# Kernel tuning notes

Hardware: AMD Instinct MI355X
Metric: run time of the kernel (lower is better)

## Reference

```python
import jax, jax.numpy as jnp
import numpy as np

T, B, D = 1024, 8, 1024
H, DH, FF = 16, 64, 4096
BG = 0.1  # GRU gating bias constant
SCALE = 1.0 / DH ** 0.5


def layer_norm(x, g, b, eps=1e-5):
    mu = jnp.mean(x, axis=-1, keepdims=True)
    var = jnp.var(x, axis=-1, keepdims=True)
    return (x - mu) * jax.lax.rsqrt(var + eps) * g + b


def gru_gate(x, y, W, U, bz):
    # W, U: [3, D, D] stacking (r, z, g) projections; bz: Uz bias
    r = jax.nn.sigmoid(y @ W[0] + x @ U[0])
    z = jax.nn.sigmoid(y @ W[1] + x @ U[1] + bz - BG)
    h = jnp.tanh(y @ W[2] + r * (x @ U[2]))
    return (1.0 - z) * x + z * h


def setup_inputs() -> dict:
    key = jax.random.key(0)
    ks = jax.random.split(key, 16)
    s = 0.02
    inp = {
        "x": jax.random.normal(ks[0], (T, B, D), jnp.float32),
        "Wq": jax.random.normal(ks[1], (D, H * DH), jnp.float32) * s,
        "Wk": jax.random.normal(ks[2], (D, H * DH), jnp.float32) * s,
        "Wv": jax.random.normal(ks[3], (D, H * DH), jnp.float32) * s,
        "Wo": jax.random.normal(ks[4], (H * DH, D), jnp.float32) * s,
        "ln1_g": jnp.ones((D,), jnp.float32),
        "ln1_b": jnp.zeros((D,), jnp.float32),
        "W1": jax.random.normal(ks[5], (D, FF), jnp.float32) * s,
        "b1": jnp.zeros((FF,), jnp.float32),
        "W2": jax.random.normal(ks[6], (FF, D), jnp.float32) * s,
        "b2": jnp.zeros((D,), jnp.float32),
        "ln2_g": jnp.ones((D,), jnp.float32),
        "ln2_b": jnp.zeros((D,), jnp.float32),
        "gate1_W": jax.random.normal(ks[7], (3, D, D), jnp.float32) * s,
        "gate1_U": jax.random.normal(ks[8], (3, D, D), jnp.float32) * s,
        "gate1_bz": jnp.zeros((D,), jnp.float32),
        "gate2_W": jax.random.normal(ks[9], (3, D, D), jnp.float32) * s,
        "gate2_U": jax.random.normal(ks[10], (3, D, D), jnp.float32) * s,
        "gate2_bz": jnp.zeros((D,), jnp.float32),
        "attn_mask": jnp.triu(jnp.ones((T, T), bool), k=1),  # causal: mask j > i
    }
    return inp


def reference(x, Wq, Wk, Wv, Wo, ln1_g, ln1_b, W1, b1, W2, b2,
              ln2_g, ln2_b, gate1_W, gate1_U, gate1_bz,
              gate2_W, gate2_U, gate2_bz, attn_mask):
    # --- multihead attention (pre_lnorm=True) ---
    xn = layer_norm(x, ln1_g, ln1_b)                     # [T,B,D]
    q = (xn @ Wq).reshape(T, B, H, DH)
    k = (xn @ Wk).reshape(T, B, H, DH)
    v = (xn @ Wv).reshape(T, B, H, DH)
    scores = jnp.einsum('ibhd,jbhd->ijbh', q, k) * SCALE  # [T,T,B,H]
    scores = jnp.where(attn_mask[:, :, None, None], -jnp.inf, scores)
    probs = jax.nn.softmax(scores, axis=1)
    attn = jnp.einsum('ijbh,jbhd->ibhd', probs, v).reshape(T, B, H * DH)
    src2 = attn @ Wo                                      # [T,B,D]
    # --- GRU gate 1 ---
    src = gru_gate(x, src2, gate1_W, gate1_U, gate1_bz)
    # --- positionwise FFN (pre_lnorm=True) ---
    sn = layer_norm(src, ln2_g, ln2_b)
    ff = jax.nn.relu(sn @ W1 + b1) @ W2 + b2
    # --- GRU gate 2 ---
    return gru_gate(src, ff, gate2_W, gate2_U, gate2_bz)
```

## Files before the change

kernel.cpp:

```cpp
#include <hip/hip_runtime.h>
#include <hip/hip_bf16.h>

#define T_  1024
#define B_  8
#define D_  1024
#define H_  16
#define DH_ 64
#define FF_ 4096
#define MROWS (T_*B_)

typedef __attribute__((ext_vector_type(8))) short short8;
typedef __attribute__((ext_vector_type(4))) float f32x4;
typedef __attribute__((ext_vector_type(4))) unsigned short us4;
typedef __attribute__((ext_vector_type(4))) unsigned int  u32x4;

__device__ __forceinline__ unsigned short f2b(float f){
  unsigned int u = __builtin_bit_cast(unsigned int, f);
  u += 0x7FFFu + ((u >> 16) & 1u);
  return (unsigned short)(u >> 16);
}
__device__ __forceinline__ float b2f(unsigned short h){
  unsigned int u = ((unsigned int)h) << 16;
  return __builtin_bit_cast(float, u);
}

__device__ __forceinline__ void glds16(const unsigned short* g, unsigned short* l){
  __builtin_amdgcn_global_load_lds(
    (const __attribute__((address_space(1))) unsigned int*)g,
    (__attribute__((address_space(3))) unsigned int*)l, 16, 0, 0);
}

enum { FRELU=1 };

__global__ __launch_bounds__(256) void gemm_bf16(
    const unsigned short* __restrict__ A1, const unsigned short* __restrict__ A2,
    int K1, long lda,
    const unsigned short* __restrict__ Bt, long ldb,
    unsigned short* __restrict__ C, long ldc,
    const float* __restrict__ bias, int K, int flags)
{
  constexpr int BM = 128, BK = 32;
  __shared__ unsigned short As[2][BM*BK];
  __shared__ unsigned short Bs[2][BM*BK];

  int t = threadIdx.x, w = t >> 6, l = t & 63;

  int nx = gridDim.x;
  int nwg = nx * gridDim.y;
  int lin = blockIdx.y*nx + blockIdx.x;
  if (!(nwg & 7)) lin = (lin & 7)*(nwg >> 3) + (lin >> 3);
  int bx = lin % nx, by = lin / nx;
  int m0 = by*BM, n0 = bx*BM;

  int arow = t >> 2, acol = (t & 3) * 8;
  const unsigned short* a1p = A1 + (long)(m0 + arow)*lda + acol;
  const unsigned short* a2p = A2 + (long)(m0 + arow)*lda + acol - K1;
  const unsigned short* bp  = Bt + (long)(n0 + arow)*ldb + acol;

  auto stage = [&](int buf, int k0){
    const unsigned short* ap = (k0 < K1) ? a1p : a2p;
    glds16(ap + k0,          &As[buf][      w*512]);
    glds16(ap + 64*lda + k0, &As[buf][2048 + w*512]);
    glds16(bp + k0,          &Bs[buf][      w*512]);
    glds16(bp + 64*ldb + k0, &Bs[buf][2048 + w*512]);
  };

  f32x4 acc[4][4];
  #pragma unroll
  for (int m=0;m<4;m++)
    #pragma unroll
    for (int n=0;n<4;n++) acc[m][n] = (f32x4){0.f,0.f,0.f,0.f};

  int wm = (w >> 1) * 64, wn = (w & 1) * 64;
  int fr = l & 15, fk = (l >> 4) * 8;
  int nk = K / BK;

  stage(0, 0);
  __syncthreads();

  for (int kt = 0; kt < nk; ++kt){
    int cur = kt & 1;
    if (kt + 1 < nk) stage(cur ^ 1, (kt+1)*BK);

    short8 af[4], bf[4];
    #pragma unroll
    for (int m=0;m<4;m++) af[m] = *(const short8*)&As[cur][(wm + m*16 + fr)*BK + fk];
    #pragma unroll
    for (int n=0;n<4;n++) bf[n] = *(const short8*)&Bs[cur][(wn + n*16 + fr)*BK + fk];
    #pragma unroll
    for (int m=0;m<4;m++)
      #pragma unroll
      for (int n=0;n<4;n++)
        acc[m][n] = __builtin_amdgcn_mfma_f32_16x16x32_bf16(af[m], bf[n], acc[m][n], 0, 0, 0);

    __syncthreads();
  }

  int r0 = m0 + wm + ((l >> 4) << 2);
  int c0 = n0 + wn + fr;
  #pragma unroll
  for (int m=0;m<4;m++)
    #pragma unroll
    for (int n=0;n<4;n++){
      int col = c0 + n*16;
      float bv = bias ? bias[col] : 0.f;
      #pragma unroll
      for (int j=0;j<4;j++){
        float v = acc[m][n][j] + bv;
        if (flags & FRELU) v = v > 0.f ? v : 0.f;
        C[(long)(r0 + m*16 + j)*ldc + col] = f2b(v);
      }
    }
}

__global__ __launch_bounds__(256) void flash_attn(
  const unsigned short* __restrict__ qkv, const unsigned short* __restrict__ vT,
  unsigned short* __restrict__ O)
{
  int p = blockIdx.x, z = blockIdx.y;
  int b = z >> 4, h = z & 15;
  const unsigned short* Vz = vT + (long)z*DH_*T_;

  __shared__ unsigned short Ks[64*64];
  __shared__ unsigned short Vs[64*64];
  __shared__ unsigned short Ps[4][32][72];

  int t = threadIdx.x, w = t >> 6, l = t & 63;
  int fr = l & 15, fg = l >> 4;
  int srow = t >> 2, sc = (t & 3) * 16;

  for (int rep = 0; rep < 2; ++rep){
    int qt = rep ? (7 - p) : p;
    int q0 = qt*128 + w*32;

    short8 qf[2][2];
    #pragma unroll
    for (int m=0;m<2;m++)
      #pragma unroll
      for (int ks=0;ks<2;ks++)
        qf[m][ks] = *(const short8*)(qkv + ((long)(q0 + m*16 + fr)*B_ + b)*3072 + h*DH_ + ks*32 + fg*8);

    f32x4 oacc[2][4];
    float mr[2][4], lr[2][4];
    #pragma unroll
    for (int m=0;m<2;m++){
      #pragma unroll
      for (int n=0;n<4;n++) oacc[m][n] = (f32x4){0.f,0.f,0.f,0.f};
      #pragma unroll
      for (int j=0;j<4;j++){ mr[m][j] = -1e30f; lr[m][j] = 0.f; }
    }

    int nkv = (qt + 1) * 2;
    for (int kt = 0; kt < nkv; ++kt){
      int kv0 = kt * 64;
      __syncthreads();
      {
        const unsigned short* kg = qkv + ((long)(kv0+srow)*B_ + b)*3072 + 1024 + h*DH_ + sc;
        const unsigned short* vg = Vz + (long)srow*T_ + kv0 + sc;
        int rb = srow*128, sw = (srow & 7) << 4;
        *(u32x4*)((char*)Ks + ((rb + sc*2     ) ^ sw)) = *(const u32x4*)(kg);
        *(u32x4*)((char*)Ks + ((rb + sc*2 + 16) ^ sw)) = *(const u32x4*)(kg + 8);
        *(u32x4*)((char*)Vs + ((rb + sc*2     ) ^ sw)) = *(const u32x4*)(vg);
        *(u32x4*)((char*)Vs + ((rb + sc*2 + 16) ^ sw)) = *(const u32x4*)(vg + 8);
      }
      __syncthreads();

      if (kv0 <= q0 + 31){
        f32x4 sacc[2][4];
        #pragma unroll
        for (int m=0;m<2;m++)
          #pragma unroll
          for (int n=0;n<4;n++) sacc[m][n] = (f32x4){0.f,0.f,0.f,0.f};
        __builtin_amdgcn_s_setprio(1);
        #pragma unroll
        for (int ks=0;ks<2;ks++){
          short8 kf[4];
          #pragma unroll
          for (int n=0;n<4;n++){
            int r = n*16 + fr;
            kf[n] = *(const short8*)((const char*)Ks + ((r*128 + ks*64 + fg*16) ^ ((r & 7) << 4)));
          }
          #pragma unroll
          for (int m=0;m<2;m++)
            #pragma unroll
            for (int n=0;n<4;n++)
              sacc[m][n] = __builtin_amdgcn_mfma_f32_16x16x32_bf16(qf[m][ks], kf[n], sacc[m][n], 0,0,0);
        }
        __builtin_amdgcn_s_setprio(0);

        #pragma unroll
        for (int m=0;m<2;m++)
          #pragma unroll
          for (int j=0;j<4;j++){
            int qg = q0 + m*16 + fg*4 + j;
            float vmax = -1e30f;
            #pragma unroll
            for (int n=0;n<4;n++){
              int kg = kv0 + n*16 + fr;
              float s = (kg <= qg) ? sacc[m][n][j]*0.125f : -1e30f;
              sacc[m][n][j] = s;
              vmax = fmaxf(vmax, s);
            }
            #pragma unroll
            for (int msk=1; msk<16; msk<<=1) vmax = fmaxf(vmax, __shfl_xor(vmax, msk));
            float mnew = fmaxf(mr[m][j], vmax);
            float sc_o = __expf(mr[m][j] - mnew);
            mr[m][j] = mnew;
            float rsum = 0.f;
            #pragma unroll
            for (int n=0;n<4;n++){
              float pv = __expf(sacc[m][n][j] - mnew);
              sacc[m][n][j] = pv;
              rsum += pv;
            }
            #pragma unroll
            for (int msk=1; msk<16; msk<<=1) rsum += __shfl_xor(rsum, msk);
            lr[m][j] = lr[m][j]*sc_o + rsum;
            #pragma unroll
            for (int n=0;n<4;n++) oacc[m][n][j] *= sc_o;
          }

        #pragma unroll
        for (int m=0;m<2;m++)
          #pragma unroll
          for (int n=0;n<4;n++)
            #pragma unroll
            for (int j=0;j<4;j++)
              Ps[w][m*16 + fg*4 + j][n*16 + fr] = f2b(sacc[m][n][j]);

        __builtin_amdgcn_s_setprio(1);
        #pragma unroll
        for (int ks=0;ks<2;ks++){
          short8 pf[2], vf[4];
          #pragma unroll
          for (int m=0;m<2;m++) pf[m] = *(const short8*)&Ps[w][m*16+fr][ks*32+fg*8];
          #pragma unroll
          for (int n=0;n<4;n++){
            int r = n*16 + fr;
            vf[n] = *(const short8*)((const char*)Vs + ((r*128 + ks*64 + fg*16) ^ ((r & 7) << 4)));
          }
          #pragma unroll
          for (int m=0;m<2;m++)
            #pragma unroll
            for (int n=0;n<4;n++)
              oacc[m][n] = __builtin_amdgcn_mfma_f32_16x16x32_bf16(pf[m], vf[n], oacc[m][n], 0,0,0);
        }
        __builtin_amdgcn_s_setprio(0);
      }
    }

    #pragma unroll
    for (int m=0;m<2;m++)
      #pragma unroll
      for (int j=0;j<4;j++){
        float inv = 1.f / lr[m][j];
        long i = q0 + m*16 + fg*4 + j;
        #pragma unroll
        for (int n=0;n<4;n++)
          O[(i*B_ + b)*(long)D_ + h*DH_ + n*16 + fr] = f2b(oacc[m][n][j] * inv);
      }
  }
}

__global__ __launch_bounds__(256) void ln_bf16(const float* __restrict__ X,
    const float* __restrict__ g, const float* __restrict__ bta,
    unsigned short* __restrict__ out)
{
  long row = blockIdx.x;
  int t = threadIdx.x;
  f32x4 xv = ((const f32x4*)(X + row*D_))[t];
  float s = xv[0]+xv[1]+xv[2]+xv[3];
  float q = xv[0]*xv[0]+xv[1]*xv[1]+xv[2]*xv[2]+xv[3]*xv[3];
  #pragma unroll
  for (int o=32;o;o>>=1){ s += __shfl_xor(s,o); q += __shfl_xor(q,o); }
  __shared__ float rs[4], rq[4];
  int w = t >> 6;
  if ((t & 63) == 0){ rs[w]=s; rq[w]=q; }
  __syncthreads();
  s = rs[0]+rs[1]+rs[2]+rs[3];
  q = rq[0]+rq[1]+rq[2]+rq[3];
  float mean = s * (1.f/D_);
  float var  = q * (1.f/D_) - mean*mean;
  float rstd = rsqrtf(var + 1e-5f);
  f32x4 gv = ((const f32x4*)g)[t];
  f32x4 bv = ((const f32x4*)bta)[t];
  us4 o;
  #pragma unroll
  for (int jj=0;jj<4;jj++) o[jj] = f2b((xv[jj]-mean)*rstd*gv[jj] + bv[jj]);
  ((us4*)(out + row*D_))[t] = o;
}

__global__ __launch_bounds__(256) void tr_f2b(const float* __restrict__ src,
    unsigned short* __restrict__ dst, int N, long ldd)
{
  __shared__ float tile[32][33];
  int k0 = blockIdx.x*32, n0 = blockIdx.y*32;
  int tx = threadIdx.x & 31, ty = threadIdx.x >> 5;
  #pragma unroll
  for (int i=0;i<4;i++)
    tile[ty+i*8][tx] = src[(long)(k0+ty+i*8)*N + n0 + tx];
  __syncthreads();
  #pragma unroll
  for (int i=0;i<4;i++)
    dst[(long)(n0+ty+i*8)*ldd + k0 + tx] = f2b(tile[tx][ty+i*8]);
}

__global__ __launch_bounds__(256) void build_vT(const unsigned short* __restrict__ vsrc,
                                                unsigned short* __restrict__ vT)
{
  __shared__ unsigned short tile[32][33];
  int z = blockIdx.z, b = z >> 4, h = z & 15;
  int t0 = blockIdx.x*32, d0 = blockIdx.y*32;
  int tx = threadIdx.x & 31, ty = threadIdx.x >> 5;
  #pragma unroll
  for (int i=0;i<4;i++)
    tile[ty+i*8][tx] = vsrc[((long)(t0+ty+i*8)*B_ + b)*3072 + h*DH_ + d0 + tx];
  __syncthreads();
  #pragma unroll
  for (int i=0;i<4;i++)
    vT[(long)z*DH_*T_ + (long)(d0+ty+i*8)*T_ + t0 + tx] = tile[tx][ty+i*8];
}

__global__ __launch_bounds__(256) void cast_f2b(const float* __restrict__ src,
                                                unsigned short* __restrict__ dst)
{
  long i = ((long)blockIdx.x*256 + threadIdx.x)*4;
  f32x4 v = *(const f32x4*)(src + i);
  us4 o;
  #pragma unroll
  for (int jj=0;jj<4;jj++) o[jj] = f2b(v[jj]);
  *(us4*)(dst + i) = o;
}

__global__ __launch_bounds__(256) void gru_combine(
  const unsigned short* __restrict__ rz,
  const unsigned short* __restrict__ ya, const unsigned short* __restrict__ xb,
  const float* __restrict__ xin, const float* __restrict__ bz,
  float* __restrict__ of, unsigned short* __restrict__ ob)
{
  long i = ((long)blockIdx.x*256 + threadIdx.x)*4;
  long row = i >> 10; int col = (int)(i & 1023);
  us4 r4 = *(const us4*)(rz + row*2048 + col);
  us4 z4 = *(const us4*)(rz + row*2048 + 1024 + col);
  us4 a4 = *(const us4*)(ya + i);
  us4 b4 = *(const us4*)(xb + i);
  f32x4 xv = *(const f32x4*)(xin + i);
  f32x4 bzv = *(const f32x4*)(bz + col);
  f32x4 o;
  #pragma unroll
  for (int jj=0;jj<4;jj++){
    float r = 1.f/(1.f + __expf(-b2f(r4[jj])));
    float z = 1.f/(1.f + __expf(-(b2f(z4[jj]) + bzv[jj] - 0.1f)));
    float h = tanhf(b2f(a4[jj]) + r*b2f(b4[jj]));
    o[jj] = (1.f - z)*xv[jj] + z*h;
  }
  *(f32x4*)(of+i) = o;
  if (ob){
    us4 q;
    #pragma unroll
    for (int jj=0;jj<4;jj++) q[jj] = f2b(o[jj]);
    *(us4*)(ob+i) = q;
  }
}

extern "C" void kernel_launch(void* const* d_in, const int* in_sizes, int n_in,
                              void* d_out, int out_size, void* d_ws, size_t ws_size,
                              hipStream_t stream)
{
  const float* x    = (const float*)d_in[0];
  const float* Wq   = (const float*)d_in[1];
  const float* Wk   = (const float*)d_in[2];
  const float* Wv   = (const float*)d_in[3];
  const float* Wo   = (const float*)d_in[4];
  const float* ln1g = (const float*)d_in[5];
  const float* ln1b = (const float*)d_in[6];
  const float* W1   = (const float*)d_in[7];
  const float* b1   = (const float*)d_in[8];
  const float* W2   = (const float*)d_in[9];
  const float* b2   = (const float*)d_in[10];
  const float* ln2g = (const float*)d_in[11];
  const float* ln2b = (const float*)d_in[12];
  const float* g1W  = (const float*)d_in[13];
  const float* g1U  = (const float*)d_in[14];
  const float* g1bz = (const float*)d_in[15];
  const float* g2W  = (const float*)d_in[16];
  const float* g2U  = (const float*)d_in[17];
  const float* g2bz = (const float*)d_in[18];
  float* out = (float*)d_out;

  const size_t MB = 1u << 20;
  if (ws_size < 144*MB) return;
  char* base = (char*)d_ws;

  unsigned short* W    = (unsigned short*)(base);
  unsigned short* x_bf = (unsigned short*)(base + 16*MB);
  unsigned short* sbf  = (unsigned short*)(base + 32*MB);
  unsigned short* src2 = (unsigned short*)(base + 48*MB);
  unsigned short* qkv  = (unsigned short*)(base + 64*MB);
  unsigned short* vT   = (unsigned short*)(base + 112*MB);
  unsigned short* attn = (unsigned short*)(base + 128*MB);
  unsigned short* xn   = attn;
  unsigned short* rz   = (unsigned short*)(base + 64*MB);
  unsigned short* yab  = (unsigned short*)(base + 96*MB);
  unsigned short* xbb  = (unsigned short*)(base + 112*MB);
  unsigned short* sn   = (unsigned short*)(base + 64*MB);
  unsigned short* ff1  = (unsigned short*)(base + 80*MB);
  unsigned short* ffb  = src2;

  const size_t E1M = 1048576;
  unsigned short* BtRZ = W;
  unsigned short* W2g  = W + 4*E1M;
  unsigned short* U2g  = W + 5*E1M;
  unsigned short* W1T  = W;
  unsigned short* W2T  = W + 4*E1M;
  unsigned short* Wqkv = W;
  unsigned short* WoT  = W + 3*E1M;

  dim3 blk(256);
  auto G = [&](const unsigned short* A1, const unsigned short* A2, int K1, long lda,
               const unsigned short* Bt, long ldb, unsigned short* C, long ldc,
               const float* bias, int M, int N, int K, int flags){
    gemm_bf16<<<dim3(N/128, M/128), blk, 0, stream>>>(A1,A2,K1,lda,Bt,ldb,C,ldc,bias,K,flags);
  };

  tr_f2b<<<dim3(32,32), blk, 0, stream>>>(Wq, Wqkv,          D_, D_);
  tr_f2b<<<dim3(32,32), blk, 0, stream>>>(Wk, Wqkv + 1*E1M,  D_, D_);
  tr_f2b<<<dim3(32,32), blk, 0, stream>>>(Wv, Wqkv + 2*E1M,  D_, D_);
  tr_f2b<<<dim3(32,32), blk, 0, stream>>>(Wo, WoT,           D_, D_);
  cast_f2b<<<dim3(MROWS), blk, 0, stream>>>(x, x_bf);

  ln_bf16<<<dim3(MROWS), blk, 0, stream>>>(x, ln1g, ln1b, xn);
  G(xn, xn, D_, D_, Wqkv, D_, qkv, 3072, nullptr, MROWS, 3072, D_, 0);
  build_vT<<<dim3(32,2,128), blk, 0, stream>>>(qkv + 2048, vT);
  flash_attn<<<dim3(4, B_*H_), blk, 0, stream>>>(qkv, vT, attn);
  G(attn, attn, D_, D_, WoT, D_, src2, D_, nullptr, MROWS, D_, D_, 0);

  tr_f2b<<<dim3(32,32), blk, 0, stream>>>(g1W + 0*E1M, BtRZ,                    D_, 2048);
  tr_f2b<<<dim3(32,32), blk, 0, stream>>>(g1U + 0*E1M, BtRZ + 1024,             D_, 2048);
  tr_f2b<<<dim3(32,32), blk, 0, stream>>>(g1W + 1*E1M, BtRZ + 1024*2048,        D_, 2048);
  tr_f2b<<<dim3(32,32), blk, 0, stream>>>(g1U + 1*E1M, BtRZ + 1024*2048 + 1024, D_, 2048);
  tr_f2b<<<dim3(32,32), blk, 0, stream>>>(g1W + 2*E1M, W2g, D_, D_);
  tr_f2b<<<dim3(32,32), blk, 0, stream>>>(g1U + 2*E1M, U2g, D_, D_);
  G(src2, x_bf, D_, D_, BtRZ, 2048, rz, 2048, nullptr, MROWS, 2048, 2048, 0);
  G(src2, src2, D_, D_, W2g, D_, yab, D_, nullptr, MROWS, D_, D_, 0);
  G(x_bf, x_bf, D_, D_, U2g, D_, xbb, D_, nullptr, MROWS, D_, D_, 0);
  gru_combine<<<dim3(MROWS), blk, 0, stream>>>(rz, yab, xbb, x, g1bz, out, sbf);

  tr_f2b<<<dim3(32,128), blk, 0, stream>>>(W1, W1T, FF_, D_);
  tr_f2b<<<dim3(128,32), blk, 0, stream>>>(W2, W2T, D_, FF_);
  ln_bf16<<<dim3(MROWS), blk, 0, stream>>>(out, ln2g, ln2b, sn);
  G(sn, sn, D_, D_, W1T, D_, ff1, FF_, b1, MROWS, FF_, D_, FRELU);
  G(ff1, ff1, FF_, FF_, W2T, FF_, ffb, D_, b2, MROWS, D_, FF_, 0);

  tr_f2b<<<dim3(32,32), blk, 0, stream>>>(g2W + 0*E1M, BtRZ,                    D_, 2048);
  tr_f2b<<<dim3(32,32), blk, 0, stream>>>(g2U + 0*E1M, BtRZ + 1024,             D_, 2048);
  tr_f2b<<<dim3(32,32), blk, 0, stream>>>(g2W + 1*E1M, BtRZ + 1024*2048,        D_, 2048);
  tr_f2b<<<dim3(32,32), blk, 0, stream>>>(g2U + 1*E1M, BtRZ + 1024*2048 + 1024, D_, 2048);
  tr_f2b<<<dim3(32,32), blk, 0, stream>>>(g2W + 2*E1M, W2g, D_, D_);
  tr_f2b<<<dim3(32,32), blk, 0, stream>>>(g2U + 2*E1M, U2g, D_, D_);
  G(ffb, sbf, D_, D_, BtRZ, 2048, rz, 2048, nullptr, MROWS, 2048, 2048, 0);
  G(ffb, ffb, D_, D_, W2g, D_, yab, D_, nullptr, MROWS, D_, D_, 0);
  G(sbf, sbf, D_, D_, U2g, D_, xbb, D_, nullptr, MROWS, D_, D_, 0);
  gru_combine<<<dim3(MROWS), blk, 0, stream>>>(rz, yab, xbb, out, g2bz, out, nullptr);
}
```

Baseline: 833.3 us.

## Add 256x256-tile triple-buffered GEMM for large-N projections

Adds a second GEMM kernel with 256x256 output tiles, 512 threads (8 waves each computing 128x64), and a three-stage LDS ring using direct global-to-LDS loads in dynamic shared memory. It is used for the wide GEMMs (QKV, GRU r/z, FFN up-projection) to raise arithmetic intensity per tile and keep more loads in flight. The extra register pressure from a 32-tile accumulator and the 96KB of LDS limit occupancy. Grids become smaller, which can hurt load balance on the N=2048 shapes.

```diff
diff --git a/kernel.cpp b/kernel.cpp
--- a/kernel.cpp
+++ b/kernel.cpp
@@ -31,6 +31,116 @@
 }
 
 enum { FRELU=1 };
+
+__global__ __launch_bounds__(512, 2) void gemm256(
+    const unsigned short* __restrict__ A1, const unsigned short* __restrict__ A2,
+    int K1, long lda,
+    const unsigned short* __restrict__ Bt, long ldb,
+    unsigned short* __restrict__ C, long ldc,
+    const float* __restrict__ bias, int K, int flags)
+{
+  constexpr int BM = 256, BK = 32;
+  extern __shared__ char L[];
+
+  int t = threadIdx.x, w = t >> 6, l = t & 63;
+
+  int nx = gridDim.x;
+  int nwg = nx * gridDim.y;
+  int lin = blockIdx.y*nx + blockIdx.x;
+  if (!(nwg & 7)) lin = (lin & 7)*(nwg >> 3) + (lin >> 3);
+  int bx = lin % nx, by = lin / nx;
+  int m0 = by*BM, n0 = bx*BM;
+
+  int srow[2], sce[2];
+  #pragma unroll
+  for (int q=0;q<2;q++){
+    int p  = q*8192 + w*1024 + l*16;
+    int sp = p ^ (((p>>6)&3)<<4);
+    srow[q] = sp >> 6;
+    sce[q]  = (sp & 63) >> 1;
+  }
+
+  auto stage = [&](int buf, int kt){
+    int k0 = kt*BK;
+    const unsigned short* ap; int ko;
+    if (k0 < K1){ ap = A1; ko = k0; } else { ap = A2; ko = k0 - K1; }
+    char* ab = L + buf*32768;
+    char* bb = ab + 16384;
+    #pragma unroll
+    for (int q=0;q<2;q++)
+      glds16(ap + (long)(m0 + srow[q])*lda + ko + sce[q],
+             (unsigned short*)(ab + q*8192 + w*1024));
+    #pragma unroll
+    for (int q=0;q<2;q++)
+      glds16(Bt + (long)(n0 + srow[q])*ldb + k0 + sce[q],
+             (unsigned short*)(bb + q*8192 + w*1024));
+  };
+
+  f32x4 acc[8][4];
+  #pragma unroll
+  for (int m=0;m<8;m++)
+    #pragma unroll
+    for (int n=0;n<4;n++) acc[m][n] = (f32x4){0.f,0.f,0.f,0.f};
+
+  int wr = w >> 2, wc = w & 3;
+  int fr = l & 15, fq = l >> 4;
+  int nk = K / BK;
+
+  stage(0, 0);
+  stage(1, 1);
+  asm volatile("s_waitcnt vmcnt(4)" ::: "memory");
+  __builtin_amdgcn_s_barrier();
+  asm volatile("" ::: "memory");
+
+  int cur = 0;
+  for (int kt = 0; kt < nk; ++kt){
+    int nxt = cur + 2; if (nxt >= 3) nxt -= 3;
+    if (kt + 2 < nk) stage(nxt, kt + 2);
+
+    const char* ab = L + cur*32768;
+    const char* bb = ab + 16384;
+    short8 af[8], bf[4];
+    #pragma unroll
+    for (int n=0;n<4;n++){
+      int r = wc*64 + n*16 + fr;
+      bf[n] = *(const short8*)(bb + ((r*64 + fq*16) ^ ((r&3)<<4)));
+    }
+    #pragma unroll
+    for (int m=0;m<8;m++){
+      int r = wr*128 + m*16 + fr;
+      af[m] = *(const short8*)(ab + ((r*64 + fq*16) ^ ((r&3)<<4)));
+    }
+    __builtin_amdgcn_s_setprio(1);
+    #pragma unroll
+    for (int m=0;m<8;m++)
+      #pragma unroll
+      for (int n=0;n<4;n++)
+        acc[m][n] = __builtin_amdgcn_mfma_f32_16x16x32_bf16(af[m], bf[n], acc[m][n], 0,0,0);
+    __builtin_amdgcn_s_setprio(0);
+
+    if (kt + 2 < nk) asm volatile("s_waitcnt vmcnt(4)" ::: "memory");
+    else             asm volatile("s_waitcnt vmcnt(0)" ::: "memory");
+    __builtin_amdgcn_s_barrier();
+    asm volatile("" ::: "memory");
+    cur += 1; if (cur >= 3) cur -= 3;
+  }
+
+  int r0 = m0 + wr*128 + (fq << 2);
+  int c0 = n0 + wc*64 + fr;
+  #pragma unroll
+  for (int m=0;m<8;m++)
+    #pragma unroll
+    for (int n=0;n<4;n++){
+      int col = c0 + n*16;
+      float bv = bias ? bias[col] : 0.f;
+      #pragma unroll
+      for (int j=0;j<4;j++){
+        float v = acc[m][n][j] + bv;
+        if (flags & FRELU) v = v > 0.f ? v : 0.f;
+        C[(long)(r0 + m*16 + j)*ldc + col] = f2b(v);
+      }
+    }
+}
 
 __global__ __launch_bounds__(256) void gemm_bf16(
     const unsigned short* __restrict__ A1, const unsigned short* __restrict__ A2,
@@ -392,6 +502,9 @@
   if (ws_size < 144*MB) return;
   char* base = (char*)d_ws;
 
+  (void)hipFuncSetAttribute((const void*)gemm256,
+                            hipFuncAttributeMaxDynamicSharedMemorySize, 98304);
+
   unsigned short* W    = (unsigned short*)(base);
   unsigned short* x_bf = (unsigned short*)(base + 16*MB);
   unsigned short* sbf  = (unsigned short*)(base + 32*MB);
@@ -422,6 +535,11 @@
                const float* bias, int M, int N, int K, int flags){
     gemm_bf16<<<dim3(N/128, M/128), blk, 0, stream>>>(A1,A2,K1,lda,Bt,ldb,C,ldc,bias,K,flags);
   };
+  auto G2 = [&](const unsigned short* A1, const unsigned short* A2, int K1, long lda,
+                const unsigned short* Bt, long ldb, unsigned short* C, long ldc,
+                const float* bias, int M, int N, int K, int flags){
+    gemm256<<<dim3(N/256, M/256), dim3(512), 98304, stream>>>(A1,A2,K1,lda,Bt,ldb,C,ldc,bias,K,flags);
+  };
 
   tr_f2b<<<dim3(32,32), blk, 0, stream>>>(Wq, Wqkv,          D_, D_);
   tr_f2b<<<dim3(32,32), blk, 0, stream>>>(Wk, Wqkv + 1*E1M,  D_, D_);
@@ -430,7 +548,7 @@
   cast_f2b<<<dim3(MROWS), blk, 0, stream>>>(x, x_bf);
 
   ln_bf16<<<dim3(MROWS), blk, 0, stream>>>(x, ln1g, ln1b, xn);
-  G(xn, xn, D_, D_, Wqkv, D_, qkv, 3072, nullptr, MROWS, 3072, D_, 0);
+  G2(xn, xn, D_, D_, Wqkv, D_, qkv, 3072, nullptr, MROWS, 3072, D_, 0);
   build_vT<<<dim3(32,2,128), blk, 0, stream>>>(qkv + 2048, vT);
   flash_attn<<<dim3(4, B_*H_), blk, 0, stream>>>(qkv, vT, attn);
   G(attn, attn, D_, D_, WoT, D_, src2, D_, nullptr, MROWS, D_, D_, 0);
@@ -441,7 +559,7 @@
   tr_f2b<<<dim3(32,32), blk, 0, stream>>>(g1U + 1*E1M, BtRZ + 1024*2048 + 1024, D_, 2048);
   tr_f2b<<<dim3(32,32), blk, 0, stream>>>(g1W + 2*E1M, W2g, D_, D_);
   tr_f2b<<<dim3(32,32), blk, 0, stream>>>(g1U + 2*E1M, U2g, D_, D_);
-  G(src2, x_bf, D_, D_, BtRZ, 2048, rz, 2048, nullptr, MROWS, 2048, 2048, 0);
+  G2(src2, x_bf, D_, D_, BtRZ, 2048, rz, 2048, nullptr, MROWS, 2048, 2048, 0);
   G(src2, src2, D_, D_, W2g, D_, yab, D_, nullptr, MROWS, D_, D_, 0);
   G(x_bf, x_bf, D_, D_, U2g, D_, xbb, D_, nullptr, MROWS, D_, D_, 0);
   gru_combine<<<dim3(MROWS), blk, 0, stream>>>(rz, yab, xbb, x, g1bz, out, sbf);
@@ -449,7 +567,7 @@
   tr_f2b<<<dim3(32,128), blk, 0, stream>>>(W1, W1T, FF_, D_);
   tr_f2b<<<dim3(128,32), blk, 0, stream>>>(W2, W2T, D_, FF_);
   ln_bf16<<<dim3(MROWS), blk, 0, stream>>>(out, ln2g, ln2b, sn);
-  G(sn, sn, D_, D_, W1T, D_, ff1, FF_, b1, MROWS, FF_, D_, FRELU);
+  G2(sn, sn, D_, D_, W1T, D_, ff1, FF_, b1, MROWS, FF_, D_, FRELU);
   G(ff1, ff1, FF_, FF_, W2T, FF_, ffb, D_, b2, MROWS, D_, FF_, 0);
 
   tr_f2b<<<dim3(32,32), blk, 0, stream>>>(g2W + 0*E1M, BtRZ,                    D_, 2048);
@@ -458,7 +576,7 @@
   tr_f2b<<<dim3(32,32), blk, 0, stream>>>(g2U + 1*E1M, BtRZ + 1024*2048 + 1024, D_, 2048);
   tr_f2b<<<dim3(32,32), blk, 0, stream>>>(g2W + 2*E1M, W2g, D_, D_);
   tr_f2b<<<dim3(32,32), blk, 0, stream>>>(g2U + 2*E1M, U2g, D_, D_);
-  G(ffb, sbf, D_, D_, BtRZ, 2048, rz, 2048, nullptr, MROWS, 2048, 2048, 0);
+  G2(ffb, sbf, D_, D_, BtRZ, 2048, rz, 2048, nullptr, MROWS, 2048, 2048, 0);
   G(ffb, ffb, D_, D_, W2g, D_, yab, D_, nullptr, MROWS, D_, D_, 0);
   G(sbf, sbf, D_, D_, U2g, D_, xbb, D_, nullptr, MROWS, D_, D_, 0);
   gru_combine<<<dim3(MROWS), blk, 0, stream>>>(rz, yab, xbb, out, g2bz, out, nullptr);
```

Measured after the change: 782.1 us. 6.1% less time.
